# Kernel tuning notes

Hardware: AMD Instinct MI355X
Metric: run time of the kernel (lower is better)

## Reference

```python
import jax, jax.numpy as jnp
import numpy as np
import math

B, L, E, H = 4, 2048, 1024, 16
HD = E // H
SIGMA = 10.0
ATTN_BIAS = 0.1  # source bug: dropout_p=0.1 is passed as attn_mask and added to scores


def setup_inputs() -> dict:
    key = jax.random.key(0)
    ks = jax.random.split(key, 6)
    return {
        "query": jax.random.normal(ks[0], (B, L, E), jnp.float32),
        "key": jax.random.normal(ks[1], (B, L, E), jnp.float32),
        "value": jax.random.normal(ks[2], (B, L, E), jnp.float32),
        "gauss": jax.random.uniform(ks[3], (B * H // 2, L), jnp.float32),
        "in_proj_weight": jax.random.normal(ks[4], (3 * E, E), jnp.float32) * (1.0 / math.sqrt(E)),
        "in_proj_bias": jnp.zeros((3 * E,), jnp.float32),
        "out_proj_weight": jax.random.normal(ks[5], (E, E), jnp.float32) * (1.0 / math.sqrt(E)),
        "out_proj_bias": jnp.zeros((E,), jnp.float32),
    }


def reference(query, key, value, gauss, in_proj_weight, in_proj_bias,
              out_proj_weight, out_proj_bias):
    # packed in-projection (q,k,v distinct tensors -> chunk weights in 3)
    wq, wk, wv = jnp.split(in_proj_weight, 3, axis=0)   # each [E, E]
    bq, bk, bv = jnp.split(in_proj_bias, 3, axis=0)
    q = query @ wq.T + bq          # [B, L, E]
    k = key @ wk.T + bk
    v = value @ wv.T + bv

    def split_heads(x):            # [B, L, E] -> [B*H, L, HD], index = b*H + h
        return x.reshape(B, L, H, HD).transpose(0, 2, 1, 3).reshape(B * H, L, HD)

    q, k, v = split_heads(q), split_heads(k), split_heads(v)
    q = q * (1.0 / math.sqrt(HD))

    attn = jnp.einsum("bnd,bmd->bnm", q, k) + ATTN_BIAS   # [B*H, L, L]
    gw = jnp.exp(-gauss * SIGMA)                          # [B*H//2, L]
    # even/odd batch rows share the same gaussian row -> pairwise broadcast
    attn = (attn.reshape(B * H // 2, 2, L, L) * gw[:, None, None, :]).reshape(B * H, L, L)
    attn = jax.nn.softmax(attn, axis=-1)

    out = jnp.einsum("bnm,bmd->bnd", attn, v)             # [B*H, L, HD]
    out = out.reshape(B, H, L, HD).transpose(0, 2, 1, 3).reshape(B, L, E)
    return out @ out_proj_weight.T + out_proj_bias        # [B, L, E]
```

## Files before the change

kernel.cpp:

```cpp
#include <hip/hip_runtime.h>
#include <stdint.h>
#include <stddef.h>


typedef __attribute__((ext_vector_type(8))) short bf16x8;
typedef __attribute__((ext_vector_type(4))) float f32x4;

__device__ __forceinline__ unsigned short f2b(float f) {
  unsigned int u = __builtin_bit_cast(unsigned int, f);
  u += 0x7FFFu + ((u >> 16) & 1u);
  return (unsigned short)(u >> 16);
}
__device__ __forceinline__ bf16x8 cvt8(f32x4 a, f32x4 b) {
  bf16x8 r;
#pragma unroll
  for (int i = 0; i < 4; ++i) { r[i] = (short)f2b(a[i]); r[4 + i] = (short)f2b(b[i]); }
  return r;
}
__device__ __forceinline__ bf16x8 pk8(f32x4 a, f32x4 b) {
  union { bf16x8 v; unsigned int w[4]; } u;
  asm("v_cvt_pk_bf16_f32 %0, %1, %2" : "=v"(u.w[0]) : "v"(a[0]), "v"(a[1]));
  asm("v_cvt_pk_bf16_f32 %0, %1, %2" : "=v"(u.w[1]) : "v"(a[2]), "v"(a[3]));
  asm("v_cvt_pk_bf16_f32 %0, %1, %2" : "=v"(u.w[2]) : "v"(b[0]), "v"(b[1]));
  asm("v_cvt_pk_bf16_f32 %0, %1, %2" : "=v"(u.w[3]) : "v"(b[2]), "v"(b[3]));
  return u.v;
}
__device__ __forceinline__ float fexp2(float x) { return __builtin_amdgcn_exp2f(x); }

#define GLD16(gp, lp) __builtin_amdgcn_global_load_lds( \
  (const __attribute__((address_space(1))) void*)(gp), \
  (__attribute__((address_space(3))) void*)(lp), 16, 0, 0)

__global__ void __launch_bounds__(256) gw_exp_kernel(const float* __restrict__ g,
                                                     float* __restrict__ gtab,
                                                     float* __restrict__ btab, int n) {
  int i = blockIdx.x * 256 + threadIdx.x;
  if (i < n) {
    const float e = __expf(g[i] * -10.0f) * 1.44269504f;
    gtab[i] = e;
    btab[i] = 0.1f * e;
  }
}

__global__ void __launch_bounds__(256) conv_bf16_kernel(
    const float* __restrict__ q, const float* __restrict__ k, const float* __restrict__ v,
    const float* __restrict__ w1, const float* __restrict__ w2,
    unsigned short* __restrict__ dst)
{
  const size_t i = ((size_t)blockIdx.x * 256 + threadIdx.x) * 8;
  const int seg = (int)(i >> 20);
  const float* s; size_t off;
  if (seg < 8)       { s = q;  off = i; }
  else if (seg < 16) { s = k;  off = i - ((size_t)8 << 20); }
  else if (seg < 24) { s = v;  off = i - ((size_t)16 << 20); }
  else if (seg < 27) { s = w1; off = i - ((size_t)24 << 20); }
  else               { s = w2; off = i - ((size_t)27 << 20); }
  const f32x4 a = *(const f32x4*)(s + off);
  const f32x4 b = *(const f32x4*)(s + off + 4);
  *(bf16x8*)(dst + i) = cvt8(a, b);
}

template<int EPI>
__global__ void __launch_bounds__(512) gemm_bt(
    const unsigned short* __restrict__ A0, const unsigned short* __restrict__ Bw,
    const float* __restrict__ bias, const float* __restrict__ gtab,
    unsigned short* __restrict__ Qo, unsigned short* __restrict__ Ko,
    unsigned short* __restrict__ Vto, float* __restrict__ Co,
    int N, int K, int nTN)
{
  const int nwg = gridDim.x;
  const int cpx = nwg >> 3;
  const int bid2 = (blockIdx.x & 7) * cpx + (blockIdx.x >> 3);
  const int tm = bid2 / nTN, tn = bid2 % nTN;

  const unsigned short* A = A0;
  if (EPI == 0) A = A0 + (size_t)(tn >> 3) * 8388608;

  __shared__ __align__(16) char lds[3][16384];

  const int tid = threadIdx.x;
  const int w = tid >> 6, l = tid & 63;
  const int lr = l & 15, lg = l >> 4;
  const size_t Kz = (size_t)K;

  auto stage = [&](int buf, int kt) {
    const int k0 = kt * 32;
    const int rl = l >> 2;
    const int cs = (l & 3) ^ ((l >> 3) & 3);
    const size_t row = (size_t)(w * 16 + rl);
    GLD16(A  + Kz * (tm * 128 + row) + k0 + cs * 8, &lds[buf][w * 1024]);
    GLD16(Bw + Kz * (tn * 128 + row) + k0 + cs * 8, &lds[buf][8192 + w * 1024]);
  };

  auto loadFrag = [&](const char* ld, int row) -> bf16x8 {
    return *(const bf16x8*)(ld + row * 64 + ((lg ^ ((row >> 1) & 3)) << 4));
  };

  f32x4 acc[4][2];
  const f32x4 zero = {0.f, 0.f, 0.f, 0.f};
#pragma unroll
  for (int i = 0; i < 4; ++i)
#pragma unroll
    for (int j = 0; j < 2; ++j) acc[i][j] = zero;

  const int wr = (w >> 2) * 64, wc = (w & 3) * 32;
  const int NT = K / 32;

  stage(0, 0);
  stage(1, 1);
  int rb = 0, wb = 2;
  for (int kt = 0; kt < NT; ++kt) {
    if (kt == NT - 1) { asm volatile("s_waitcnt vmcnt(0)" ::: "memory"); }
    else              { asm volatile("s_waitcnt vmcnt(2)" ::: "memory"); }
    __builtin_amdgcn_sched_barrier(0);
    __builtin_amdgcn_s_barrier();
    __builtin_amdgcn_sched_barrier(0);
    if (kt + 2 < NT) stage(wb, kt + 2);
    const char* la = lds[rb];
    const char* lb = lds[rb] + 8192;
    bf16x8 af[4], bfr[2];
#pragma unroll
    for (int mi = 0; mi < 4; ++mi) af[mi] = loadFrag(la, wr + mi * 16 + lr);
#pragma unroll
    for (int ni = 0; ni < 2; ++ni) bfr[ni] = loadFrag(lb, wc + ni * 16 + lr);
#pragma unroll
    for (int mi = 0; mi < 4; ++mi)
#pragma unroll
      for (int ni = 0; ni < 2; ++ni)
        acc[mi][ni] = __builtin_amdgcn_mfma_f32_16x16x32_bf16(
            af[mi], bfr[ni], acc[mi][ni], 0, 0, 0);
    rb = (rb == 2) ? 0 : rb + 1;
    wb = (wb == 2) ? 0 : wb + 1;
  }

  if (EPI == 0 && tn >= 16) {
    __syncthreads();
    char* T = &lds[0][0];
#pragma unroll
    for (int ni = 0; ni < 2; ++ni) {
      const int cnl = wc + ni * 16 + lr;
      const float bv = bias[tn * 128 + cnl];
#pragma unroll
      for (int mi = 0; mi < 4; ++mi)
#pragma unroll
        for (int r = 0; r < 4; ++r) {
          const int rml = wr + mi * 16 + lg * 4 + r;
          const int byte = cnl * 256 + (((rml * 2)) ^ ((cnl & 3) << 5));
          *(unsigned short*)(T + byte) = f2b(acc[mi][ni][r] + bv);
        }
    }
    __syncthreads();
    const int bbase = (tm >> 4) * 16 + (tn - 16) * 2;
    const size_t ncol = (size_t)(tm & 15) * 128;
#pragma unroll
    for (int rep = 0; rep < 4; ++rep) {
      const int U = rep * 512 + tid;
      const int row = U >> 4;
      const int un = U & 15;
      const bf16x8 vv = *(const bf16x8*)(T + row * 256 + ((un * 16) ^ ((row & 3) << 5)));
      const int bh = bbase + (row >> 6);
      const int d = row & 63;
      *(bf16x8*)(Vto + ((size_t)bh * 64 + d) * 2048 + ncol + un * 8) = vv;
    }
  } else {
#pragma unroll
    for (int ni = 0; ni < 2; ++ni) {
      const int cn = tn * 128 + wc + ni * 16 + lr;
      const float bv = bias[cn];
      const int j = cn & 1023;
      const float* gK = nullptr;
      if constexpr (EPI == 0) {
        if ((cn >> 10) == 1) {
          const int bh_ = (tm >> 4) * 16 + (j >> 6);
          gK = gtab + (size_t)(bh_ >> 1) * 2048;
        }
      }
#pragma unroll
      for (int mi = 0; mi < 4; ++mi) {
        const int rm0 = tm * 128 + wr + mi * 16 + lg * 4;
        f32x4 g4;
        if constexpr (EPI == 0) {
          if (gK) g4 = *(const f32x4*)&gK[rm0 & 2047];
        }
#pragma unroll
        for (int r = 0; r < 4; ++r) {
          const int rm = rm0 + r;
          const float val = acc[mi][ni][r] + bv;
          if constexpr (EPI == 0) {
            const int which = cn >> 10;
            const int bh = (rm >> 11) * 16 + (j >> 6);
            const int d = j & 63;
            const int n = rm & 2047;
            if (which == 0) Qo[((size_t)bh * 2048 + n) * 64 + d] = f2b(val * 0.125f);
            else            Ko[((size_t)bh * 2048 + n) * 64 + d] = f2b(val * g4[r]);
          } else {
            Co[(size_t)rm * N + cn] = val;
          }
        }
      }
    }
  }
}

__global__ void __launch_bounds__(256, 2) attn_kernel(
    const unsigned short* __restrict__ Q, const unsigned short* __restrict__ Kf,
    const unsigned short* __restrict__ Vt, const float* __restrict__ btab,
    unsigned short* __restrict__ O)
{
  const int bid2 = (blockIdx.x & 7) * 64 + (blockIdx.x >> 3);
  const int bh = bid2 >> 3;
  const int qb = bid2 & 7;
  const int tid = threadIdx.x;
  const int w = tid >> 6, l = tid & 63;
  const int lr = l & 15, lg = l >> 4;

  __shared__ __align__(16) unsigned short Kl[2][64 * 64];
  __shared__ __align__(16) unsigned short Vl[2][64 * 64];

  const int qrow = qb * 256 + w * 64 + lr;
  const unsigned short* qp = &Q[((size_t)bh * 2048 + qrow) * 64];
  bf16x8 aq[4][2];
#pragma unroll
  for (int st = 0; st < 4; ++st) {
    aq[st][0] = *(const bf16x8*)&qp[st * 16 * 64 + lg * 8];
    aq[st][1] = *(const bf16x8*)&qp[st * 16 * 64 + 32 + lg * 8];
  }

  const f32x4 zero = {0.f, 0.f, 0.f, 0.f};
  f32x4 accO[4][4];
  f32x4 lsum[4];
#pragma unroll
  for (int st = 0; st < 4; ++st) {
    lsum[st] = zero;
#pragma unroll
    for (int dt = 0; dt < 4; ++dt) accO[st][dt] = zero;
  }

  const short oneb = (short)0x3F80;
  const bf16x8 vones = {oneb, oneb, oneb, oneb, oneb, oneb, oneb, oneb};

  int off[4][2];
#pragma unroll
  for (int mt = 0; mt < 4; ++mt)
#pragma unroll
    for (int c = 0; c < 2; ++c) {
      const int rr = mt * 16 + lr;
      off[mt][c] = rr * 128 + ((((c << 2) + lg) ^ (rr & 7)) << 4);
    }

  const int rr0 = w * 8 + (l >> 3);
  const int cc = ((l & 7) ^ (rr0 & 7)) * 8;
  const int kk0 = (rr0 & 35) | ((rr0 & 12) << 1) | ((rr0 & 16) >> 2);
  const unsigned short* kSrc = &Kf[((size_t)bh * 2048 + kk0) * 64 + cc];
  const unsigned short* vSrc = &Vt[((size_t)bh * 64 + rr0) * 2048 + cc];

  auto stageKV = [&](int buf) {
    GLD16(kSrc,             &Kl[buf][w * 512]);
    GLD16(kSrc + 32 * 64,   &Kl[buf][(w + 4) * 512]);
    GLD16(vSrc,             &Vl[buf][w * 512]);
    GLD16(vSrc + 32 * 2048, &Vl[buf][(w + 4) * 512]);
    kSrc += 64 * 64;
    vSrc += 64;
  };

  const float* brow = &btab[(size_t)(bh >> 1) * 2048];

  stageKV(0);
  for (int t = 0; t < 32; ++t) {
    __syncthreads();
    if (t + 1 < 32) stageKV((t + 1) & 1);
    const char* kl = (const char*)Kl[t & 1];
    const char* vl = (const char*)Vl[t & 1];

    bf16x8 ap[4][2];
#pragma unroll
    for (int half = 0; half < 2; ++half) {
      f32x4 s[4][2];
      __builtin_amdgcn_s_setprio(1);
#pragma unroll
      for (int mh = 0; mh < 2; ++mh) {
        const int mt = half * 2 + mh;
        const bf16x8 bk0 = *(const bf16x8*)(kl + off[mt][0]);
        const bf16x8 bk1 = *(const bf16x8*)(kl + off[mt][1]);
        const f32x4 b4 = *(const f32x4*)&brow[t * 64 + (half << 5) + (lg << 3) + (mh << 2)];
#pragma unroll
        for (int st = 0; st < 4; ++st) {
          f32x4 a = __builtin_amdgcn_mfma_f32_16x16x32_bf16(bk0, aq[st][0], b4, 0, 0, 0);
          a = __builtin_amdgcn_mfma_f32_16x16x32_bf16(bk1, aq[st][1], a, 0, 0, 0);
          s[st][mh] = a;
        }
      }
      __builtin_amdgcn_s_setprio(0);
#pragma unroll
      for (int st = 0; st < 4; ++st) {
#pragma unroll
        for (int mh = 0; mh < 2; ++mh)
#pragma unroll
          for (int r = 0; r < 4; ++r) s[st][mh][r] = fexp2(s[st][mh][r]);
        ap[st][half] = pk8(s[st][0], s[st][1]);
      }
    }

    __builtin_amdgcn_s_setprio(1);
#pragma unroll
    for (int st = 0; st < 4; ++st) {
      lsum[st] = __builtin_amdgcn_mfma_f32_16x16x32_bf16(ap[st][0], vones, lsum[st], 0, 0, 0);
      lsum[st] = __builtin_amdgcn_mfma_f32_16x16x32_bf16(ap[st][1], vones, lsum[st], 0, 0, 0);
    }
#pragma unroll
    for (int dt = 0; dt < 4; ++dt) {
      const bf16x8 bv0 = *(const bf16x8*)(vl + off[dt][0]);
      const bf16x8 bv1 = *(const bf16x8*)(vl + off[dt][1]);
#pragma unroll
      for (int st = 0; st < 4; ++st) {
        f32x4 a = accO[st][dt];
        a = __builtin_amdgcn_mfma_f32_16x16x32_bf16(ap[st][0], bv0, a, 0, 0, 0);
        a = __builtin_amdgcn_mfma_f32_16x16x32_bf16(ap[st][1], bv1, a, 0, 0, 0);
        accO[st][dt] = a;
      }
    }
    __builtin_amdgcn_s_setprio(0);
  }

  const int oc0 = (bh & 15) * 64;
#pragma unroll
  for (int st = 0; st < 4; ++st) {
    const int orow0 = (bh >> 4) * 2048 + qb * 256 + w * 64 + st * 16 + lg * 4;
    f32x4 rc;
#pragma unroll
    for (int r = 0; r < 4; ++r) rc[r] = 1.0f / lsum[st][r];
#pragma unroll
    for (int dt = 0; dt < 4; ++dt)
#pragma unroll
      for (int r = 0; r < 4; ++r)
        O[(size_t)(orow0 + r) * 1024 + oc0 + dt * 16 + lr] = f2b(accO[st][dt][r] * rc[r]);
  }
}

extern "C" void kernel_launch(void* const* d_in, const int* in_sizes, int n_in,
                              void* d_out, int out_size, void* d_ws, size_t ws_size,
                              hipStream_t stream) {
  (void)in_sizes; (void)n_in; (void)out_size; (void)ws_size;
  const float* query = (const float*)d_in[0];
  const float* key_  = (const float*)d_in[1];
  const float* value = (const float*)d_in[2];
  const float* gauss = (const float*)d_in[3];
  const float* ipw   = (const float*)d_in[4];
  const float* ipb   = (const float*)d_in[5];
  const float* opw   = (const float*)d_in[6];
  const float* opb   = (const float*)d_in[7];

  char* ws = (char*)d_ws;
  unsigned short* Xbf = (unsigned short*)ws;
  unsigned short* W1  = Xbf + ((size_t)24 << 20);
  unsigned short* W2  = Xbf + ((size_t)27 << 20);
  unsigned short* AO  = Xbf;
  unsigned short* Qf  = Xbf + ((size_t)28 << 20);
  unsigned short* Kf  = Qf + (size_t)64 * 2048 * 64;
  unsigned short* Vt  = Kf + (size_t)64 * 2048 * 64;
  float*          gtab = (float*)(Vt + (size_t)64 * 2048 * 64);
  float*          btab = gtab + 32 * 2048;

  gw_exp_kernel<<<256, 256, 0, stream>>>(gauss, gtab, btab, 32 * 2048);

  conv_bf16_kernel<<<14336, 256, 0, stream>>>(query, key_, value, ipw, opw, Xbf);

  gemm_bt<0><<<64 * 24, 512, 0, stream>>>(
      Xbf, W1, ipb, gtab, Qf, Kf, Vt, nullptr, 3072, 1024, 24);

  attn_kernel<<<512, 256, 0, stream>>>(Qf, Kf, Vt, btab, AO);

  gemm_bt<1><<<64 * 8, 512, 0, stream>>>(
      AO, W2, opb, nullptr, nullptr, nullptr, nullptr, (float*)d_out, 1024, 1024, 8);
}
```

Baseline: 204.9 us.

## Rework projection GEMMs into 128x256 tiles with 64-deep K double-buffered pipeline

Both projection GEMMs move from 128x128 tiles with a K=32 triple buffer to 128x256 tiles with a K=64 double buffer of 48KB stages. Loads for the next stage are interleaved between half-tile MFMA groups, and MFMA sections run at raised wave priority via setprio. Each wave now holds a 64x64 accumulator, which raises arithmetic intensity per LDS read and halves the block count. The cost is higher register and LDS pressure, and fewer blocks, which can leave CUs underfilled: the out-projection launches only 256 blocks.

```diff
diff --git a/kernel.cpp b/kernel.cpp
--- a/kernel.cpp
+++ b/kernel.cpp
@@ -30,6 +30,14 @@
 #define GLD16(gp, lp) __builtin_amdgcn_global_load_lds( \
   (const __attribute__((address_space(1))) void*)(gp), \
   (__attribute__((address_space(3))) void*)(lp), 16, 0, 0)
+
+#define FBAR() do { \
+  asm volatile("" ::: "memory"); \
+  __builtin_amdgcn_sched_barrier(0); \
+  __builtin_amdgcn_s_barrier(); \
+  __builtin_amdgcn_sched_barrier(0); \
+  asm volatile("" ::: "memory"); \
+} while (0)
 
 __global__ void __launch_bounds__(256) gw_exp_kernel(const float* __restrict__ g,
                                                      float* __restrict__ gtab,
@@ -61,7 +69,7 @@
 }
 
 template<int EPI>
-__global__ void __launch_bounds__(512) gemm_bt(
+__global__ void __launch_bounds__(512, 2) gemm8p(
     const unsigned short* __restrict__ A0, const unsigned short* __restrict__ Bw,
     const float* __restrict__ bias, const float* __restrict__ gtab,
     unsigned short* __restrict__ Qo, unsigned short* __restrict__ Ko,
@@ -74,110 +82,168 @@
   const int tm = bid2 / nTN, tn = bid2 % nTN;
 
   const unsigned short* A = A0;
-  if (EPI == 0) A = A0 + (size_t)(tn >> 3) * 8388608;
-
-  __shared__ __align__(16) char lds[3][16384];
+  if (EPI == 0) A = A0 + (size_t)(tn >> 2) * 8388608;
+
+  __shared__ __align__(16) char lds[2][49152];
 
   const int tid = threadIdx.x;
   const int w = tid >> 6, l = tid & 63;
   const int lr = l & 15, lg = l >> 4;
+  const int wm = w >> 2, wn = w & 3;
   const size_t Kz = (size_t)K;
 
-  auto stage = [&](int buf, int kt) {
-    const int k0 = kt * 32;
-    const int rl = l >> 2;
-    const int cs = (l & 3) ^ ((l >> 3) & 3);
-    const size_t row = (size_t)(w * 16 + rl);
-    GLD16(A  + Kz * (tm * 128 + row) + k0 + cs * 8, &lds[buf][w * 1024]);
-    GLD16(Bw + Kz * (tn * 128 + row) + k0 + cs * 8, &lds[buf][8192 + w * 1024]);
-  };
-
-  auto loadFrag = [&](const char* ld, int row) -> bf16x8 {
-    return *(const bf16x8*)(ld + row * 64 + ((lg ^ ((row >> 1) & 3)) << 4));
-  };
-
-  f32x4 acc[4][2];
+  const int r0 = tid >> 3;
+  const int sch = (((tid & 7) ^ ((tid >> 3) & 7)) << 3);
+  const size_t arow0 = (size_t)(tm * 128 + r0);
+  const size_t brow0 = (size_t)(tn * 256 + r0);
+
+  auto stA = [&](int s, int k0) {
+    GLD16(A + arow0 * Kz + k0 + sch,        &lds[s][tid * 16]);
+    GLD16(A + (arow0 + 64) * Kz + k0 + sch, &lds[s][8192 + tid * 16]);
+  };
+  auto stB = [&](int s, int h, int k0) {
+    const size_t rb = brow0 + h * 128;
+    GLD16(Bw + rb * Kz + k0 + sch,        &lds[s][16384 + h * 16384 + tid * 16]);
+    GLD16(Bw + (rb + 64) * Kz + k0 + sch, &lds[s][16384 + h * 16384 + 8192 + tid * 16]);
+  };
+
+  int offA[4][2], offB[4][2];
+#pragma unroll
+  for (int m = 0; m < 4; ++m) {
+    const int ra = wm * 64 + m * 16 + lr;
+#pragma unroll
+    for (int kk = 0; kk < 2; ++kk)
+      offA[m][kk] = ra * 128 + ((((kk << 2) | lg) ^ (ra & 7)) << 4);
+  }
+#pragma unroll
+  for (int n = 0; n < 4; ++n) {
+    const int br = wn * 64 + n * 16 + lr;
+    const int lrow = br & 127;
+#pragma unroll
+    for (int kk = 0; kk < 2; ++kk)
+      offB[n][kk] = 16384 + (br >> 7) * 16384 + lrow * 128 +
+                    ((((kk << 2) | lg) ^ (lrow & 7)) << 4);
+  }
+
+  f32x4 acc[4][4];
   const f32x4 zero = {0.f, 0.f, 0.f, 0.f};
 #pragma unroll
   for (int i = 0; i < 4; ++i)
 #pragma unroll
-    for (int j = 0; j < 2; ++j) acc[i][j] = zero;
-
-  const int wr = (w >> 2) * 64, wc = (w & 3) * 32;
-  const int NT = K / 32;
-
-  stage(0, 0);
-  stage(1, 1);
-  int rb = 0, wb = 2;
-  for (int kt = 0; kt < NT; ++kt) {
-    if (kt == NT - 1) { asm volatile("s_waitcnt vmcnt(0)" ::: "memory"); }
-    else              { asm volatile("s_waitcnt vmcnt(2)" ::: "memory"); }
+    for (int j = 0; j < 4; ++j) acc[i][j] = zero;
+
+  bf16x8 af[2][2], bf[4][2];
+
+  auto loadA = [&](const char* Ls, int mh) {
+#pragma unroll
+    for (int mm = 0; mm < 2; ++mm)
+#pragma unroll
+      for (int kk = 0; kk < 2; ++kk)
+        af[mm][kk] = *(const bf16x8*)(Ls + offA[mh * 2 + mm][kk]);
+  };
+  auto loadB = [&](const char* Ls) {
+#pragma unroll
+    for (int n = 0; n < 4; ++n)
+#pragma unroll
+      for (int kk = 0; kk < 2; ++kk)
+        bf[n][kk] = *(const bf16x8*)(Ls + offB[n][kk]);
+  };
+  auto mfmaq = [&](int mh) {
+    asm volatile("s_waitcnt lgkmcnt(0)" ::: "memory");
     __builtin_amdgcn_sched_barrier(0);
-    __builtin_amdgcn_s_barrier();
-    __builtin_amdgcn_sched_barrier(0);
-    if (kt + 2 < NT) stage(wb, kt + 2);
-    const char* la = lds[rb];
-    const char* lb = lds[rb] + 8192;
-    bf16x8 af[4], bfr[2];
-#pragma unroll
-    for (int mi = 0; mi < 4; ++mi) af[mi] = loadFrag(la, wr + mi * 16 + lr);
-#pragma unroll
-    for (int ni = 0; ni < 2; ++ni) bfr[ni] = loadFrag(lb, wc + ni * 16 + lr);
-#pragma unroll
-    for (int mi = 0; mi < 4; ++mi)
-#pragma unroll
-      for (int ni = 0; ni < 2; ++ni)
-        acc[mi][ni] = __builtin_amdgcn_mfma_f32_16x16x32_bf16(
-            af[mi], bfr[ni], acc[mi][ni], 0, 0, 0);
-    rb = (rb == 2) ? 0 : rb + 1;
-    wb = (wb == 2) ? 0 : wb + 1;
-  }
-
-  if (EPI == 0 && tn >= 16) {
+    __builtin_amdgcn_s_setprio(1);
+#pragma unroll
+    for (int mm = 0; mm < 2; ++mm)
+#pragma unroll
+      for (int n = 0; n < 4; ++n) {
+        f32x4 a = acc[mh * 2 + mm][n];
+        a = __builtin_amdgcn_mfma_f32_16x16x32_bf16(af[mm][0], bf[n][0], a, 0, 0, 0);
+        a = __builtin_amdgcn_mfma_f32_16x16x32_bf16(af[mm][1], bf[n][1], a, 0, 0, 0);
+        acc[mh * 2 + mm][n] = a;
+      }
+    __builtin_amdgcn_s_setprio(0);
+  };
+
+  const char* L0 = (const char*)lds[0];
+  const char* L1 = (const char*)lds[1];
+
+  stA(0, 0); stB(0, 0, 0); stB(0, 1, 0);
+
+  const int NI = K / 128;
+  for (int i = 0; i < NI; ++i) {
+    const int k1 = i * 128 + 64;
+    const int k2 = i * 128 + 128;
+    stA(1, k1); stB(1, 0, k1);
+    asm volatile("s_waitcnt vmcnt(4)" ::: "memory");
+    FBAR();
+    loadA(L0, 0); loadB(L0);
+    mfmaq(0);
+    FBAR();
+    stB(1, 1, k1);
+    loadA(L0, 1);
+    mfmaq(1);
+    FBAR();
+    if (i + 1 < NI) {
+      stA(0, k2); stB(0, 0, k2);
+      asm volatile("s_waitcnt vmcnt(4)" ::: "memory");
+    } else {
+      asm volatile("s_waitcnt vmcnt(0)" ::: "memory");
+    }
+    FBAR();
+    loadA(L1, 0); loadB(L1);
+    mfmaq(0);
+    FBAR();
+    if (i + 1 < NI) stB(0, 1, k2);
+    loadA(L1, 1);
+    mfmaq(1);
+    FBAR();
+  }
+
+  if (EPI == 0 && (tn >> 2) == 2) {
     __syncthreads();
     char* T = &lds[0][0];
 #pragma unroll
-    for (int ni = 0; ni < 2; ++ni) {
-      const int cnl = wc + ni * 16 + lr;
-      const float bv = bias[tn * 128 + cnl];
-#pragma unroll
-      for (int mi = 0; mi < 4; ++mi)
+    for (int n = 0; n < 4; ++n) {
+      const int cnl = wn * 64 + n * 16 + lr;
+      const float bv = bias[tn * 256 + cnl];
+      const int sw = (cnl & 7) << 4;
+#pragma unroll
+      for (int m = 0; m < 4; ++m)
 #pragma unroll
         for (int r = 0; r < 4; ++r) {
-          const int rml = wr + mi * 16 + lg * 4 + r;
-          const int byte = cnl * 256 + (((rml * 2)) ^ ((cnl & 3) << 5));
-          *(unsigned short*)(T + byte) = f2b(acc[mi][ni][r] + bv);
+          const int rml = wm * 64 + m * 16 + lg * 4 + r;
+          *(unsigned short*)(T + cnl * 256 + ((rml * 2) ^ sw)) = f2b(acc[m][n][r] + bv);
         }
     }
     __syncthreads();
-    const int bbase = (tm >> 4) * 16 + (tn - 16) * 2;
+    const int bbase = (tm >> 4) * 16 + (tn - 8) * 4;
     const size_t ncol = (size_t)(tm & 15) * 128;
 #pragma unroll
-    for (int rep = 0; rep < 4; ++rep) {
+    for (int rep = 0; rep < 8; ++rep) {
       const int U = rep * 512 + tid;
       const int row = U >> 4;
       const int un = U & 15;
-      const bf16x8 vv = *(const bf16x8*)(T + row * 256 + ((un * 16) ^ ((row & 3) << 5)));
+      const bf16x8 vv = *(const bf16x8*)(T + row * 256 + ((un * 16) ^ ((row & 7) << 4)));
       const int bh = bbase + (row >> 6);
       const int d = row & 63;
       *(bf16x8*)(Vto + ((size_t)bh * 64 + d) * 2048 + ncol + un * 8) = vv;
     }
   } else {
 #pragma unroll
-    for (int ni = 0; ni < 2; ++ni) {
-      const int cn = tn * 128 + wc + ni * 16 + lr;
+    for (int n = 0; n < 4; ++n) {
+      const int cn = tn * 256 + wn * 64 + n * 16 + lr;
       const float bv = bias[cn];
       const int j = cn & 1023;
       const float* gK = nullptr;
       if constexpr (EPI == 0) {
-        if ((cn >> 10) == 1) {
+        if ((tn >> 2) == 1) {
           const int bh_ = (tm >> 4) * 16 + (j >> 6);
           gK = gtab + (size_t)(bh_ >> 1) * 2048;
         }
       }
 #pragma unroll
-      for (int mi = 0; mi < 4; ++mi) {
-        const int rm0 = tm * 128 + wr + mi * 16 + lg * 4;
+      for (int m = 0; m < 4; ++m) {
+        const int rm0 = tm * 128 + wm * 64 + m * 16 + lg * 4;
         f32x4 g4;
         if constexpr (EPI == 0) {
           if (gK) g4 = *(const f32x4*)&gK[rm0 & 2047];
@@ -185,14 +251,13 @@
 #pragma unroll
         for (int r = 0; r < 4; ++r) {
           const int rm = rm0 + r;
-          const float val = acc[mi][ni][r] + bv;
+          const float val = acc[m][n][r] + bv;
           if constexpr (EPI == 0) {
-            const int which = cn >> 10;
             const int bh = (rm >> 11) * 16 + (j >> 6);
             const int d = j & 63;
-            const int n = rm & 2047;
-            if (which == 0) Qo[((size_t)bh * 2048 + n) * 64 + d] = f2b(val * 0.125f);
-            else            Ko[((size_t)bh * 2048 + n) * 64 + d] = f2b(val * g4[r]);
+            const int nr = rm & 2047;
+            if ((tn >> 2) == 0) Qo[((size_t)bh * 2048 + nr) * 64 + d] = f2b(val * 0.125f);
+            else                Ko[((size_t)bh * 2048 + nr) * 64 + d] = f2b(val * g4[r]);
           } else {
             Co[(size_t)rm * N + cn] = val;
           }
@@ -365,11 +430,11 @@
 
   conv_bf16_kernel<<<14336, 256, 0, stream>>>(query, key_, value, ipw, opw, Xbf);
 
-  gemm_bt<0><<<64 * 24, 512, 0, stream>>>(
-      Xbf, W1, ipb, gtab, Qf, Kf, Vt, nullptr, 3072, 1024, 24);
+  gemm8p<0><<<64 * 12, 512, 0, stream>>>(
+      Xbf, W1, ipb, gtab, Qf, Kf, Vt, nullptr, 3072, 1024, 12);
 
   attn_kernel<<<512, 256, 0, stream>>>(Qf, Kf, Vt, btab, AO);
 
-  gemm_bt<1><<<64 * 8, 512, 0, stream>>>(
-      AO, W2, opb, nullptr, nullptr, nullptr, nullptr, (float*)d_out, 1024, 1024, 8);
-}
+  gemm8p<1><<<64 * 4, 512, 0, stream>>>(
+      AO, W2, opb, nullptr, nullptr, nullptr, nullptr, (float*)d_out, 1024, 1024, 4);
+}
```

Result: faster. 197.3 us (-3.7%).
